# Performance work log

Hardware: AMD Instinct MI355X
Metric: run time of the kernel (lower is better)

Reference implementation:

```python
import jax, jax.numpy as jnp
import numpy as np
from jax import lax

V = 50000      # node_num
LN = 128       # feat_dim
S = 16         # stat_dim
E = 500000     # n_edges
T = 3          # propagation steps
MU = 0.9


def setup_inputs() -> dict:
    key = jax.random.key(0)
    ks = jax.random.split(key, 10)
    X_Node = jax.random.randint(ks[0], (E,), 0, V, dtype=jnp.int32)
    X_Neis = jax.random.randint(ks[1], (E,), 0, V, dtype=jnp.int32)
    dg_list = jax.random.randint(ks[2], (E,), 1, 64, dtype=jnp.int32)
    emb = jax.random.normal(ks[3], (V, LN), dtype=jnp.float32) * 0.1
    xi_w = jax.random.normal(ks[4], (2 * LN, S * S), dtype=jnp.float32) * (1.0 / np.sqrt(2 * LN))
    xi_b = jnp.zeros((S * S,), dtype=jnp.float32)
    rou_w = jax.random.normal(ks[5], (LN, S), dtype=jnp.float32) * (1.0 / np.sqrt(LN))
    rou_b = jnp.zeros((S,), dtype=jnp.float32)
    lin_w = jax.random.normal(ks[6], (LN + S, 3), dtype=jnp.float32) * (1.0 / np.sqrt(LN + S))
    lin_b = jnp.zeros((3,), dtype=jnp.float32)
    return {"X_Node": X_Node, "X_Neis": X_Neis, "dg_list": dg_list,
            "emb": emb, "xi_w": xi_w, "xi_b": xi_b,
            "rou_w": rou_w, "rou_b": rou_b, "lin_w": lin_w, "lin_b": lin_b}


def reference(X_Node, X_Neis, dg_list, emb, xi_w, xi_b, rou_w, rou_b, lin_w, lin_b):
    # edge features: concat(src embed, nbr embed) -> [E, 2*ln]
    Xn = emb[X_Node]                                  # [E, ln]
    X = jnp.concatenate([Xn, emb[X_Neis]], axis=1)    # [E, 2*ln]
    dg = dg_list.astype(emb.dtype)
    # Hw: A = Xi(X)*mu/s/dg  (constant across iterations; torch recomputes, same math)
    A = jnp.tanh(X @ xi_w + xi_b).reshape(-1, S, S)   # [E, s, s]
    A = A * (MU / S) / dg[:, None, None]
    b = jnp.tanh(Xn @ rou_w + rou_b)                  # [E, s]

    states0 = jnp.zeros((V, S), dtype=emb.dtype)

    def step(states, _):
        H = states[X_Node]                            # [E, s] gather
        H = jnp.einsum('est,et->es', A, H) + b        # per-edge small matvec
        states = jax.ops.segment_sum(H, X_Neis, num_segments=V)  # scatter-sum (AggrSum)
        return states, None

    states, _ = lax.scan(step, states0, None, length=T)
    logits = jnp.concatenate([emb, states], axis=1) @ lin_w + lin_b  # [V, 3]
    return jax.nn.softmax(logits, axis=1)
```

## Files before the change

kernel.cpp:

```cpp
#include <hip/hip_runtime.h>
#include <hip/hip_bf16.h>
#include <hip/hip_fp16.h>

#define LN_F 128

typedef __attribute__((ext_vector_type(8))) __bf16 bf16x8;
typedef __attribute__((ext_vector_type(4))) float f32x4;
typedef __attribute__((ext_vector_type(2))) _Float16 half2_t;
typedef __attribute__((ext_vector_type(2))) __fp16 fp16x2_t;

__device__ __forceinline__ unsigned short f2bf(float f) {
    unsigned u = __float_as_uint(f);
    u = u + 0x7FFFu + ((u >> 16) & 1u);
    return (unsigned short)(u >> 16);
}
__device__ __forceinline__ float tanh_polyc(float x) {
    x = fminf(1.2f, fmaxf(-1.2f, x));
    float t = x * x;
    float p = fmaf(t, -0.05396825397f, 0.13333333333f);
    p = fmaf(t, p, -0.33333333333f);
    p = fmaf(t, p, 1.0f);
    return x * p;
}
__device__ __forceinline__ float bflo(unsigned u) { return __uint_as_float(u << 16); }
__device__ __forceinline__ float bfhi(unsigned u) { return __uint_as_float(u & 0xffff0000u); }

__device__ __forceinline__ unsigned f2e5(float x) {
    unsigned short u = __half_as_ushort(__float2half(x));
    u = (unsigned short)(u + 0x7F + ((u >> 8) & 1));
    return (unsigned)(u >> 8) & 0xFFu;
}
__device__ __forceinline__ half2_t u2h2(unsigned w) {
    union { unsigned u; half2_t h; } c; c.u = w; return c.h;
}
__device__ __forceinline__ unsigned h2u(half2_t h) {
    union { half2_t h; unsigned u; } c; c.h = h; return c.u;
}
__device__ __forceinline__ unsigned pkrtz_u32(float lo, float hi) {
    union { fp16x2_t h; unsigned u; } c;
    c.h = __builtin_amdgcn_cvt_pkrtz(lo, hi);
    return c.u;
}
__device__ __forceinline__ half2_t tanh_pk(half2_t x) {
    const half2_t c2 = {(_Float16)(2.0f / 15.0f), (_Float16)(2.0f / 15.0f)};
    const half2_t c1 = {(_Float16)(-1.0f / 3.0f), (_Float16)(-1.0f / 3.0f)};
    const half2_t one = {(_Float16)1.0f, (_Float16)1.0f};
    half2_t t = x * x;
    half2_t p = t * c2 + c1;
    p = t * p + one;
    return x * p;
}

__global__ void k_conv(const float* __restrict__ emb, const float* __restrict__ xiw,
                       const float* __restrict__ rw, const int* __restrict__ Xe,
                       unsigned short* __restrict__ embb, unsigned short* __restrict__ WcT,
                       unsigned short* __restrict__ rouT, int* __restrict__ cnt,
                       float* __restrict__ B1, float* __restrict__ stB,
                       float* __restrict__ stA, int V, int E) {
    int t = blockIdx.x * blockDim.x + threadIdx.x;
    int n_emb = V * 16;
    if (t < n_emb) {
        const float4* s = (const float4*)emb;
        float4 a = s[t * 2], b = s[t * 2 + 1];
        uint4 o;
        o.x = (unsigned)f2bf(a.x) | ((unsigned)f2bf(a.y) << 16);
        o.y = (unsigned)f2bf(a.z) | ((unsigned)f2bf(a.w) << 16);
        o.z = (unsigned)f2bf(b.x) | ((unsigned)f2bf(b.y) << 16);
        o.w = (unsigned)f2bf(b.z) | ((unsigned)f2bf(b.w) << 16);
        ((uint4*)embb)[t] = o;
        B1[t] = 0.f;
        stB[t] = 0.f;
        stA[t] = 0.f;
    } else if (t < n_emb + 512 * 16) {
        int t2 = t - n_emb;
        int cp = t2 >> 4, g = t2 & 15;
        unsigned short u[8];
#pragma unroll
        for (int j = 0; j < 8; ++j) {
            int k = g * 8 + j;
            float w = (cp < 256) ? xiw[k * 256 + cp] : xiw[(128 + k) * 256 + (cp - 256)];
            u[j] = f2bf(w);
        }
        uint4 o;
        o.x = (unsigned)u[0] | ((unsigned)u[1] << 16);
        o.y = (unsigned)u[2] | ((unsigned)u[3] << 16);
        o.z = (unsigned)u[4] | ((unsigned)u[5] << 16);
        o.w = (unsigned)u[6] | ((unsigned)u[7] << 16);
        ((uint4*)WcT)[cp * 16 + (g ^ (cp & 7))] = o;
    } else if (t < n_emb + 512 * 16 + 256) {
        int t2 = t - n_emb - 512 * 16;
        int c = t2 >> 4, g = t2 & 15;
        unsigned short u[8];
#pragma unroll
        for (int j = 0; j < 8; ++j) u[j] = f2bf(rw[(g * 8 + j) * 16 + c]);
        uint4 o;
        o.x = (unsigned)u[0] | ((unsigned)u[1] << 16);
        o.y = (unsigned)u[2] | ((unsigned)u[3] << 16);
        o.z = (unsigned)u[4] | ((unsigned)u[5] << 16);
        o.w = (unsigned)u[6] | ((unsigned)u[7] << 16);
        ((uint4*)rouT)[c * 16 + (g ^ (c & 7))] = o;
    }
    if (t < E) atomicAdd(&cnt[Xe[t]], 1);
}

__global__ __launch_bounds__(256) void k_scan1(const int* __restrict__ cnt,
                                               int* __restrict__ rp,
                                               int* __restrict__ bsum, int V) {
    __shared__ int ls[256];
    int b = blockIdx.x, t = threadIdx.x;
    int i = b * 256 + t;
    int val = (i < V) ? cnt[i] : 0;
    ls[t] = val;
    __syncthreads();
    for (int off = 1; off < 256; off <<= 1) {
        int x = (t >= off) ? ls[t - off] : 0;
        __syncthreads();
        ls[t] += x;
        __syncthreads();
    }
    if (i < V) rp[i] = ls[t] - val;
    if (t == 255) bsum[b] = ls[255];
}

__global__ __launch_bounds__(256) void k_scan2(const int* __restrict__ bsum,
                                               int* __restrict__ boff, int NB) {
    __shared__ int ls[256];
    int t = threadIdx.x;
    int val = (t < NB) ? bsum[t] : 0;
    ls[t] = val;
    __syncthreads();
    for (int off = 1; off < 256; off <<= 1) {
        int x = (t >= off) ? ls[t - off] : 0;
        __syncthreads();
        ls[t] += x;
        __syncthreads();
    }
    if (t < NB) boff[t] = ls[t] - val;
}

__global__ __launch_bounds__(256) void k_permute(
    const int* __restrict__ Xn, const int* __restrict__ Xe,
    const int* __restrict__ dg, const int* __restrict__ rp,
    const int* __restrict__ boff, int* __restrict__ c2,
    uint2* __restrict__ erec, int E, int Epad, int V) {
    int part = blockIdx.x & 7;
    int sub = blockIdx.x >> 3;
    int nsub = gridDim.x >> 3;
    int per = (V + 7) >> 3;
    int vlo = part * per;
    int vhi = min(V, vlo + per);
    int stride = nsub * 256;
    for (int e = sub * 256 + threadIdx.x; e < E; e += stride) {
        int nb = Xe[e];
        if (nb >= vlo && nb < vhi) {
            int pos = rp[nb] + boff[nb >> 8] + atomicAdd(&c2[nb], 1);
            uint2 r;
            r.x = (unsigned)Xn[e] | ((unsigned)nb << 16);
            r.y = (unsigned)__float_as_int(0.05625f / (float)dg[e]);
            erec[pos] = r;
        }
    }
    if (part == 7) {
        for (int e = E + sub * 256 + threadIdx.x; e < Epad; e += stride)
            erec[e] = make_uint2(0u, 0u);
    }
}

__global__ __launch_bounds__(512) void k_U(
    const unsigned short* __restrict__ embb, const uint4* __restrict__ WcT,
    const uint4* __restrict__ rouT, const float* __restrict__ xib,
    const float* __restrict__ roub,
    unsigned* __restrict__ U8, unsigned* __restrict__ U28,
    float* __restrict__ bnode, int V) {
    __shared__ uint4 sB[2048];
    __shared__ uint4 sR[256];
    const int half = blockIdx.y;
    for (int i = threadIdx.x; i < 2048; i += 512) sB[i] = WcT[half * 2048 + i];
    if (half == 0 && threadIdx.x < 256) sR[threadIdx.x] = rouT[threadIdx.x];
    __syncthreads();

    const int wave = threadIdx.x >> 6, lane = threadIdx.x & 63;
    const int j = lane & 15, kg = lane >> 4;
    const int wbase = blockIdx.x * 512 + wave * 64;

    int nv[4];
#pragma unroll
    for (int g = 0; g < 4; ++g) nv[g] = min(wbase + g * 16 + j, V - 1);

    f32x4 acc[8][4] = {};
    f32x4 accb[4] = {};
#pragma unroll
    for (int kc = 0; kc < 4; ++kc) {
        bf16x8 bf[4];
#pragma unroll
        for (int g = 0; g < 4; ++g)
            bf[g] = *(const bf16x8*)(embb + (size_t)nv[g] * 128 + kc * 32 + kg * 8);
        int swz = (kc * 4 + kg) ^ (j & 7);
#pragma unroll
        for (int ct = 0; ct < 8; ++ct) {
            bf16x8 afr = ((const bf16x8*)sB)[(ct * 16 + j) * 16 + swz];
#pragma unroll
            for (int g = 0; g < 4; ++g)
                acc[ct][g] = __builtin_amdgcn_mfma_f32_16x16x32_bf16(afr, bf[g], acc[ct][g], 0, 0, 0);
        }
        if (half == 0) {
            bf16x8 rfr = ((const bf16x8*)sR)[j * 16 + swz];
#pragma unroll
            for (int g = 0; g < 4; ++g)
                accb[g] = __builtin_amdgcn_mfma_f32_16x16x32_bf16(rfr, bf[g], accb[g], 0, 0, 0);
        }
    }

#pragma unroll
    for (int ct = 0; ct < 8; ++ct) {
        int c0 = half * 128 + ct * 16 + kg * 4;
        float4 bias = (half < 2) ? ((const float4*)xib)[c0 >> 2]
                                 : make_float4(0.f, 0.f, 0.f, 0.f);
#pragma unroll
        for (int g = 0; g < 4; ++g) {
            int node = wbase + g * 16 + j;
            if (node < V) {
                const f32x4 a = acc[ct][g];
                float v0 = a[0] + bias.x, v1 = a[1] + bias.y;
                float v2 = a[2] + bias.z, v3 = a[3] + bias.w;
                unsigned pk = f2e5(v0) | (f2e5(v1) << 8) | (f2e5(v2) << 16) | (f2e5(v3) << 24);
                if (half < 2) U8[node * 64 + (c0 >> 2)] = pk;
                else          U28[node * 64 + ((c0 - 256) >> 2)] = pk;
            }
        }
    }
    if (half == 0) {
        float4 rb4 = ((const float4*)roub)[kg];
#pragma unroll
        for (int g = 0; g < 4; ++g) {
            int node = wbase + g * 16 + j;
            if (node < V) {
                float4 bo;
                bo.x = tanh_polyc(accb[g][0] + rb4.x);
                bo.y = tanh_polyc(accb[g][1] + rb4.y);
                bo.z = tanh_polyc(accb[g][2] + rb4.z);
                bo.w = tanh_polyc(accb[g][3] + rb4.w);
                *(float4*)(bnode + (size_t)node * 16 + kg * 4) = bo;
            }
        }
    }
}

__global__ __launch_bounds__(256) void k_B1e(
    const float* __restrict__ bnode, const uint2* __restrict__ erec,
    float* __restrict__ B1, float* __restrict__ stB, float* __restrict__ stA,
    int E, int Epad) {
    int wid = (blockIdx.x * 256 + threadIdx.x) >> 6;
    int wbase = wid * 64;
    if (wbase >= Epad) return;
    int lane = threadIdx.x & 63;
    int g = lane >> 4, s = lane & 15, lbase = g * 16;
    int sbase = wbase + lbase;

    int em = wbase + lane;
    unsigned rx = erec[em].x;
    int my_u = (int)(rx & 0xFFFFu);
    int d_own = (int)(rx >> 16);
    int d_nxt = (int)(((const unsigned*)erec)[2 * min(em + 1, Epad - 1)] >> 16);
    unsigned long long flags = __ballot(d_own != d_nxt);

    int cur = __shfl(d_own, lbase, 64);
    float acc = 0.f;
#pragma unroll 4
    for (int j = 0; j < 16; ++j) {
        int p = sbase + j;
        int u = __shfl(my_u, lbase + j, 64);
        float v = bnode[(size_t)u * 16 + s];
        acc += (p < E) ? v : 0.f;
        bool flush = ((flags >> (lbase + j)) & 1ull) || (j == 15);
        if (flush) {
            size_t idx = (size_t)cur * 16 + s;
            atomicAdd(&B1[idx], acc);
            atomicAdd(&stB[idx], acc);
            atomicAdd(&stA[idx], acc);
            acc = 0.f;
            if (j < 15) cur = __shfl(d_nxt, lbase + j, 64);
        }
    }
}

__global__ __launch_bounds__(256) void k_prop_e(
    const unsigned* __restrict__ U8, const unsigned* __restrict__ U28,
    const uint2* __restrict__ erec, const float* __restrict__ sp,
    float* __restrict__ sn, int Epad) {
    int wid = (blockIdx.x * 256 + threadIdx.x) >> 6;
    int wbase = wid * 64;
    if (wbase >= Epad) return;
    int lane = threadIdx.x & 63;
    int g = lane >> 4, s = lane & 15, lbase = g * 16;

    int em = wbase + lane;
    uint2 myr = erec[em];
    int my_u = (int)(myr.x & 0xFFFFu);
    int d_own = (int)(myr.x >> 16);
    int d_nxt = (int)(((const unsigned*)erec)[2 * min(em + 1, Epad - 1)] >> 16);
    unsigned long long flags = __ballot(d_own != d_nxt);

    int cur = __shfl(d_own, lbase, 64);
    half2_t u2h[8];
    {
        uint4 r = ((const uint4*)U28)[cur * 16 + s];
        unsigned wr[4] = {r.x, r.y, r.z, r.w};
#pragma unroll
        for (int q = 0; q < 4; ++q) {
            u2h[2 * q]     = u2h2(__builtin_amdgcn_perm(wr[q], 0u, 0x05000400u));
            u2h[2 * q + 1] = u2h2(__builtin_amdgcn_perm(wr[q], 0u, 0x07000600u));
        }
    }

    float acc = 0.f;
#pragma unroll 4
    for (int j = 0; j < 16; ++j) {
        int u = __shfl(my_u, lbase + j, 64);
        float sc = __int_as_float(__shfl((int)myr.y, lbase + j, 64));
        uint4 q1 = ((const uint4*)U8)[u * 16 + s];
        float2 hf = *(const float2*)(sp + (size_t)u * 16 + (s & 7) * 2);
        unsigned h2 = pkrtz_u32(hf.x, hf.y);
        unsigned wq[4] = {q1.x, q1.y, q1.z, q1.w};
        float sum = 0.f;
#pragma unroll
        for (int q = 0; q < 4; ++q) {
            half2_t x0 = u2h2(__builtin_amdgcn_perm(wq[q], 0u, 0x05000400u)) + u2h[2 * q];
            half2_t x1 = u2h2(__builtin_amdgcn_perm(wq[q], 0u, 0x07000600u)) + u2h[2 * q + 1];
            half2_t r0 = tanh_pk(x0);
            half2_t r1 = tanh_pk(x1);
            unsigned hm0 = __shfl(h2, lbase + 2 * q, 64);
            unsigned hm1 = __shfl(h2, lbase + 2 * q + 1, 64);
            sum = __builtin_amdgcn_fdot2(r0, u2h2(hm0), sum, false);
            sum = __builtin_amdgcn_fdot2(r1, u2h2(hm1), sum, false);
        }
        acc = fmaf(sc, sum, acc);
        bool flush = ((flags >> (lbase + j)) & 1ull) || (j == 15);
        if (flush) {
            atomicAdd(&sn[(size_t)cur * 16 + s], acc);
            acc = 0.f;
            if (j < 15) {
                cur = __shfl(d_nxt, lbase + j, 64);
                uint4 r = ((const uint4*)U28)[cur * 16 + s];
                unsigned wr[4] = {r.x, r.y, r.z, r.w};
#pragma unroll
                for (int q = 0; q < 4; ++q) {
                    u2h[2 * q]     = u2h2(__builtin_amdgcn_perm(wr[q], 0u, 0x05000400u));
                    u2h[2 * q + 1] = u2h2(__builtin_amdgcn_perm(wr[q], 0u, 0x07000600u));
                }
            }
        }
    }
}

__global__ void k_final(const unsigned short* __restrict__ embb, const float* __restrict__ st,
                        const float* __restrict__ lw, const float* __restrict__ lb,
                        float* __restrict__ out, int nv) {
    __shared__ float sw[435];
    for (int i = threadIdx.x; i < 435; i += 256) sw[i] = (i < 432) ? lw[i] : lb[i - 432];
    __syncthreads();
    int t = blockIdx.x * blockDim.x + threadIdx.x;
    int v = t >> 4, j = t & 15;
    if (v >= nv) return;
    const uint4 q = *(const uint4*)(embb + (size_t)v * 128 + j * 8);
    unsigned uu[4] = {q.x, q.y, q.z, q.w};
    float a0 = 0.f, a1 = 0.f, a2 = 0.f;
#pragma unroll
    for (int m = 0; m < 4; ++m) {
        int i = j * 8 + 2 * m;
        float x0 = bflo(uu[m]), x1 = bfhi(uu[m]);
        a0 += x0 * sw[i * 3] + x1 * sw[(i + 1) * 3];
        a1 += x0 * sw[i * 3 + 1] + x1 * sw[(i + 1) * 3 + 1];
        a2 += x0 * sw[i * 3 + 2] + x1 * sw[(i + 1) * 3 + 2];
    }
    float xs = st[(size_t)v * 16 + j];
    a0 += xs * sw[(128 + j) * 3]; a1 += xs * sw[(128 + j) * 3 + 1]; a2 += xs * sw[(128 + j) * 3 + 2];
#pragma unroll
    for (int m = 1; m < 16; m <<= 1) {
        a0 += __shfl_xor(a0, m, 64);
        a1 += __shfl_xor(a1, m, 64);
        a2 += __shfl_xor(a2, m, 64);
    }
    if (j == 0) {
        a0 += sw[432]; a1 += sw[433]; a2 += sw[434];
        float mx = fmaxf(a0, fmaxf(a1, a2));
        float e0 = __expf(a0 - mx), e1 = __expf(a1 - mx), e2 = __expf(a2 - mx);
        float inv = 1.f / (e0 + e1 + e2);
        out[(size_t)v * 3 + 0] = e0 * inv;
        out[(size_t)v * 3 + 1] = e1 * inv;
        out[(size_t)v * 3 + 2] = e2 * inv;
    }
}

extern "C" void kernel_launch(void* const* d_in, const int* in_sizes, int n_in,
                              void* d_out, int out_size, void* d_ws, size_t ws_size,
                              hipStream_t stream) {
    const int*   Xn  = (const int*)d_in[0];
    const int*   Xe  = (const int*)d_in[1];
    const int*   dg  = (const int*)d_in[2];
    const float* emb = (const float*)d_in[3];
    const float* xiw = (const float*)d_in[4];
    const float* xib = (const float*)d_in[5];
    const float* rw  = (const float*)d_in[6];
    const float* rb  = (const float*)d_in[7];
    const float* lw  = (const float*)d_in[8];
    const float* lb  = (const float*)d_in[9];
    float* out = (float*)d_out;
    const int E = in_sizes[0];
    const int V = in_sizes[3] / LN_F;
    const int NB = (V + 255) / 256;
    const int Epad = (E + 63) & ~63;

    char* p = (char*)d_ws;
    auto carve = [&](size_t bytes) {
        char* q = p; p += (bytes + 255) & ~(size_t)255; return q;
    };
    int*   cnt   = (int*)carve((size_t)V * 4);
    int*   c2    = (int*)carve((size_t)V * 4);
    size_t zero_bytes = (size_t)(p - (char*)cnt);
    float* B1    = (float*)carve((size_t)V * 16 * 4);
    unsigned short* embb = (unsigned short*)carve((size_t)V * 128 * 2);
    unsigned* U8    = (unsigned*)carve((size_t)V * 256);
    unsigned* U28   = (unsigned*)carve((size_t)V * 256);
    uint4* WcT   = (uint4*)carve(512 * 16 * 16);
    uint4* rouT  = (uint4*)carve(4096);
    float* bnode = (float*)carve((size_t)V * 16 * 4);
    float* stB   = (float*)carve((size_t)V * 16 * 4);
    float* stA   = (float*)carve((size_t)V * 16 * 4);
    int*   rp    = (int*)carve((size_t)(V + 1) * 4);
    int*   bsum  = (int*)carve(256 * 4);
    int*   boff  = (int*)carve(256 * 4);
    uint2* erec  = (uint2*)carve((size_t)Epad * 8);

    hipMemsetAsync(cnt, 0, zero_bytes, stream);

    {
        int nconv = V * 16 + 512 * 16 + 256;
        int ntot = nconv > E ? nconv : E;
        k_conv<<<(ntot + 255) / 256, 256, 0, stream>>>(
            emb, xiw, rw, Xe, embb, (unsigned short*)WcT, (unsigned short*)rouT,
            cnt, B1, stB, stA, V, E);
    }

    k_scan1<<<NB, 256, 0, stream>>>(cnt, rp, bsum, V);
    k_scan2<<<1, 256, 0, stream>>>(bsum, boff, NB);

    k_permute<<<1024, 256, 0, stream>>>(Xn, Xe, dg, rp, boff, c2, erec, E, Epad, V);

    {
        dim3 g((V + 511) / 512, 4);
        k_U<<<g, 512, 0, stream>>>(embb, WcT, rouT, xib, rb, U8, U28, bnode, V);
    }

    const int pblocks = (Epad / 64 + 3) / 4;

    k_B1e<<<pblocks, 256, 0, stream>>>(bnode, erec, B1, stB, stA, E, Epad);

    k_prop_e<<<pblocks, 256, 0, stream>>>(U8, U28, erec, B1, stB, Epad);

    k_prop_e<<<pblocks, 256, 0, stream>>>(U8, U28, erec, stB, stA, Epad);

    k_final<<<((size_t)V * 16 + 255) / 256, 256, 0, stream>>>(embb, stA, lw, lb, out, V);
}
```

Measured before the change: 178.6 us.

## Fuse block-offset scan and edge permute into node GEMM kernel launch

Merges k_scan2, k_permute and k_U into one heterogeneous launch. The first UBLOCKS blocks compute the per-node GEMM. The remaining 512 blocks each redo the small block-sum scan in shared memory and then scatter edges into CSR order. This removes two kernel launches and lets the memory-bound permute run alongside the MFMA-bound GEMM. In exchange every permute block repeats the scan, the shared-memory footprint grows for all blocks, and permute now uses 512-thread blocks.

```diff
diff --git a/kernel.cpp b/kernel.cpp
--- a/kernel.cpp
+++ b/kernel.cpp
@@ -32,9 +32,6 @@
 }
 __device__ __forceinline__ half2_t u2h2(unsigned w) {
     union { unsigned u; half2_t h; } c; c.u = w; return c.h;
-}
-__device__ __forceinline__ unsigned h2u(half2_t h) {
-    union { half2_t h; unsigned u; } c; c.h = h; return c.u;
 }
 __device__ __forceinline__ unsigned pkrtz_u32(float lo, float hi) {
     union { fp16x2_t h; unsigned u; } c;
@@ -122,126 +119,125 @@
     if (t == 255) bsum[b] = ls[255];
 }
 
-__global__ __launch_bounds__(256) void k_scan2(const int* __restrict__ bsum,
-                                               int* __restrict__ boff, int NB) {
-    __shared__ int ls[256];
-    int t = threadIdx.x;
-    int val = (t < NB) ? bsum[t] : 0;
-    ls[t] = val;
-    __syncthreads();
-    for (int off = 1; off < 256; off <<= 1) {
-        int x = (t >= off) ? ls[t - off] : 0;
-        __syncthreads();
-        ls[t] += x;
-        __syncthreads();
-    }
-    if (t < NB) boff[t] = ls[t] - val;
-}
-
-__global__ __launch_bounds__(256) void k_permute(
-    const int* __restrict__ Xn, const int* __restrict__ Xe,
-    const int* __restrict__ dg, const int* __restrict__ rp,
-    const int* __restrict__ boff, int* __restrict__ c2,
-    uint2* __restrict__ erec, int E, int Epad, int V) {
-    int part = blockIdx.x & 7;
-    int sub = blockIdx.x >> 3;
-    int nsub = gridDim.x >> 3;
-    int per = (V + 7) >> 3;
-    int vlo = part * per;
-    int vhi = min(V, vlo + per);
-    int stride = nsub * 256;
-    for (int e = sub * 256 + threadIdx.x; e < E; e += stride) {
-        int nb = Xe[e];
-        if (nb >= vlo && nb < vhi) {
-            int pos = rp[nb] + boff[nb >> 8] + atomicAdd(&c2[nb], 1);
-            uint2 r;
-            r.x = (unsigned)Xn[e] | ((unsigned)nb << 16);
-            r.y = (unsigned)__float_as_int(0.05625f / (float)dg[e]);
-            erec[pos] = r;
-        }
-    }
-    if (part == 7) {
-        for (int e = E + sub * 256 + threadIdx.x; e < Epad; e += stride)
-            erec[e] = make_uint2(0u, 0u);
-    }
-}
-
-__global__ __launch_bounds__(512) void k_U(
+__global__ __launch_bounds__(512) void k_Uperm(
     const unsigned short* __restrict__ embb, const uint4* __restrict__ WcT,
     const uint4* __restrict__ rouT, const float* __restrict__ xib,
     const float* __restrict__ roub,
     unsigned* __restrict__ U8, unsigned* __restrict__ U28,
-    float* __restrict__ bnode, int V) {
-    __shared__ uint4 sB[2048];
-    __shared__ uint4 sR[256];
-    const int half = blockIdx.y;
-    for (int i = threadIdx.x; i < 2048; i += 512) sB[i] = WcT[half * 2048 + i];
-    if (half == 0 && threadIdx.x < 256) sR[threadIdx.x] = rouT[threadIdx.x];
-    __syncthreads();
-
-    const int wave = threadIdx.x >> 6, lane = threadIdx.x & 63;
-    const int j = lane & 15, kg = lane >> 4;
-    const int wbase = blockIdx.x * 512 + wave * 64;
-
-    int nv[4];
-#pragma unroll
-    for (int g = 0; g < 4; ++g) nv[g] = min(wbase + g * 16 + j, V - 1);
-
-    f32x4 acc[8][4] = {};
-    f32x4 accb[4] = {};
-#pragma unroll
-    for (int kc = 0; kc < 4; ++kc) {
-        bf16x8 bf[4];
-#pragma unroll
-        for (int g = 0; g < 4; ++g)
-            bf[g] = *(const bf16x8*)(embb + (size_t)nv[g] * 128 + kc * 32 + kg * 8);
-        int swz = (kc * 4 + kg) ^ (j & 7);
+    float* __restrict__ bnode,
+    const int* __restrict__ Xn, const int* __restrict__ Xe,
+    const int* __restrict__ dg, const int* __restrict__ rp,
+    const int* __restrict__ bsum, int* __restrict__ c2,
+    uint2* __restrict__ erec,
+    int V, int E, int Epad, int NB, int UBLOCKS) {
+    if ((int)blockIdx.x < UBLOCKS) {
+        __shared__ uint4 sB[2048];
+        __shared__ uint4 sR[256];
+        const int half = blockIdx.x & 3;
+        for (int i = threadIdx.x; i < 2048; i += 512) sB[i] = WcT[half * 2048 + i];
+        if (half == 0 && threadIdx.x < 256) sR[threadIdx.x] = rouT[threadIdx.x];
+        __syncthreads();
+
+        const int wave = threadIdx.x >> 6, lane = threadIdx.x & 63;
+        const int j = lane & 15, kg = lane >> 4;
+        const int wbase = (blockIdx.x >> 2) * 512 + wave * 64;
+
+        int nv[4];
+#pragma unroll
+        for (int g = 0; g < 4; ++g) nv[g] = min(wbase + g * 16 + j, V - 1);
+
+        f32x4 acc[8][4] = {};
+        f32x4 accb[4] = {};
+#pragma unroll
+        for (int kc = 0; kc < 4; ++kc) {
+            bf16x8 bf[4];
+#pragma unroll
+            for (int g = 0; g < 4; ++g)
+                bf[g] = *(const bf16x8*)(embb + (size_t)nv[g] * 128 + kc * 32 + kg * 8);
+            int swz = (kc * 4 + kg) ^ (j & 7);
+#pragma unroll
+            for (int ct = 0; ct < 8; ++ct) {
+                bf16x8 afr = ((const bf16x8*)sB)[(ct * 16 + j) * 16 + swz];
+#pragma unroll
+                for (int g = 0; g < 4; ++g)
+                    acc[ct][g] = __builtin_amdgcn_mfma_f32_16x16x32_bf16(afr, bf[g], acc[ct][g], 0, 0, 0);
+            }
+            if (half == 0) {
+                bf16x8 rfr = ((const bf16x8*)sR)[j * 16 + swz];
+#pragma unroll
+                for (int g = 0; g < 4; ++g)
+                    accb[g] = __builtin_amdgcn_mfma_f32_16x16x32_bf16(rfr, bf[g], accb[g], 0, 0, 0);
+            }
+        }
+
 #pragma unroll
         for (int ct = 0; ct < 8; ++ct) {
-            bf16x8 afr = ((const bf16x8*)sB)[(ct * 16 + j) * 16 + swz];
-#pragma unroll
-            for (int g = 0; g < 4; ++g)
-                acc[ct][g] = __builtin_amdgcn_mfma_f32_16x16x32_bf16(afr, bf[g], acc[ct][g], 0, 0, 0);
+            int c0 = half * 128 + ct * 16 + kg * 4;
+            float4 bias = (half < 2) ? ((const float4*)xib)[c0 >> 2]
+                                     : make_float4(0.f, 0.f, 0.f, 0.f);
+#pragma unroll
+            for (int g = 0; g < 4; ++g) {
+                int node = wbase + g * 16 + j;
+                if (node < V) {
+                    const f32x4 a = acc[ct][g];
+                    float v0 = a[0] + bias.x, v1 = a[1] + bias.y;
+                    float v2 = a[2] + bias.z, v3 = a[3] + bias.w;
+                    unsigned pk = f2e5(v0) | (f2e5(v1) << 8) | (f2e5(v2) << 16) | (f2e5(v3) << 24);
+                    if (half < 2) U8[node * 64 + (c0 >> 2)] = pk;
+                    else          U28[node * 64 + ((c0 - 256) >> 2)] = pk;
+                }
+            }
         }
         if (half == 0) {
-            bf16x8 rfr = ((const bf16x8*)sR)[j * 16 + swz];
-#pragma unroll
-            for (int g = 0; g < 4; ++g)
-                accb[g] = __builtin_amdgcn_mfma_f32_16x16x32_bf16(rfr, bf[g], accb[g], 0, 0, 0);
-        }
-    }
-
-#pragma unroll
-    for (int ct = 0; ct < 8; ++ct) {
-        int c0 = half * 128 + ct * 16 + kg * 4;
-        float4 bias = (half < 2) ? ((const float4*)xib)[c0 >> 2]
-                                 : make_float4(0.f, 0.f, 0.f, 0.f);
-#pragma unroll
-        for (int g = 0; g < 4; ++g) {
-            int node = wbase + g * 16 + j;
-            if (node < V) {
-                const f32x4 a = acc[ct][g];
-                float v0 = a[0] + bias.x, v1 = a[1] + bias.y;
-                float v2 = a[2] + bias.z, v3 = a[3] + bias.w;
-                unsigned pk = f2e5(v0) | (f2e5(v1) << 8) | (f2e5(v2) << 16) | (f2e5(v3) << 24);
-                if (half < 2) U8[node * 64 + (c0 >> 2)] = pk;
-                else          U28[node * 64 + ((c0 - 256) >> 2)] = pk;
-            }
-        }
-    }
-    if (half == 0) {
-        float4 rb4 = ((const float4*)roub)[kg];
-#pragma unroll
-        for (int g = 0; g < 4; ++g) {
-            int node = wbase + g * 16 + j;
-            if (node < V) {
-                float4 bo;
-                bo.x = tanh_polyc(accb[g][0] + rb4.x);
-                bo.y = tanh_polyc(accb[g][1] + rb4.y);
-                bo.z = tanh_polyc(accb[g][2] + rb4.z);
-                bo.w = tanh_polyc(accb[g][3] + rb4.w);
-                *(float4*)(bnode + (size_t)node * 16 + kg * 4) = bo;
-            }
+            float4 rb4 = ((const float4*)roub)[kg];
+#pragma unroll
+            for (int g = 0; g < 4; ++g) {
+                int node = wbase + g * 16 + j;
+                if (node < V) {
+                    float4 bo;
+                    bo.x = tanh_polyc(accb[g][0] + rb4.x);
+                    bo.y = tanh_polyc(accb[g][1] + rb4.y);
+                    bo.z = tanh_polyc(accb[g][2] + rb4.z);
+                    bo.w = tanh_polyc(accb[g][3] + rb4.w);
+                    *(float4*)(bnode + (size_t)node * 16 + kg * 4) = bo;
+                }
+            }
+        }
+    } else {
+        __shared__ int lb[256];
+        int t = threadIdx.x;
+        int val = 0;
+        if (t < 256) { val = (t < NB) ? bsum[t] : 0; lb[t] = val; }
+        __syncthreads();
+        for (int off = 1; off < 256; off <<= 1) {
+            int x = (t < 256 && t >= off) ? lb[t - off] : 0;
+            __syncthreads();
+            if (t < 256) lb[t] += x;
+            __syncthreads();
+        }
+        if (t < 256) lb[t] -= val;
+        __syncthreads();
+
+        int pb = blockIdx.x - UBLOCKS;
+        int part = pb & 7, sub = pb >> 3;
+        int nsub = ((int)gridDim.x - UBLOCKS) >> 3;
+        int per = (V + 7) >> 3;
+        int vlo = part * per;
+        int vhi = min(V, vlo + per);
+        int stride = nsub * 512;
+        for (int e = sub * 512 + t; e < E; e += stride) {
+            int nb = Xe[e];
+            if (nb >= vlo && nb < vhi) {
+                int pos = rp[nb] + lb[nb >> 8] + atomicAdd(&c2[nb], 1);
+                uint2 r;
+                r.x = (unsigned)Xn[e] | ((unsigned)nb << 16);
+                r.y = (unsigned)__float_as_int(0.05625f / (float)dg[e]);
+                erec[pos] = r;
+            }
+        }
+        if (part == 7) {
+            for (int e = E + sub * 512 + t; e < Epad; e += stride)
+                erec[e] = make_uint2(0u, 0u);
         }
     }
 }
@@ -429,7 +425,6 @@
     float* stA   = (float*)carve((size_t)V * 16 * 4);
     int*   rp    = (int*)carve((size_t)(V + 1) * 4);
     int*   bsum  = (int*)carve(256 * 4);
-    int*   boff  = (int*)carve(256 * 4);
     uint2* erec  = (uint2*)carve((size_t)Epad * 8);
 
     hipMemsetAsync(cnt, 0, zero_bytes, stream);
@@ -443,13 +438,13 @@
     }
 
     k_scan1<<<NB, 256, 0, stream>>>(cnt, rp, bsum, V);
-    k_scan2<<<1, 256, 0, stream>>>(bsum, boff, NB);
-
-    k_permute<<<1024, 256, 0, stream>>>(Xn, Xe, dg, rp, boff, c2, erec, E, Epad, V);
 
     {
-        dim3 g((V + 511) / 512, 4);
-        k_U<<<g, 512, 0, stream>>>(embb, WcT, rouT, xib, rb, U8, U28, bnode, V);
+        int UBLOCKS = ((V + 511) / 512) * 4;
+        int PB = 512;
+        k_Uperm<<<UBLOCKS + PB, 512, 0, stream>>>(
+            embb, WcT, rouT, xib, rb, U8, U28, bnode,
+            Xn, Xe, dg, rp, bsum, c2, erec, V, E, Epad, NB, UBLOCKS);
     }
 
     const int pblocks = (Epad / 64 + 3) / 4;
```

After: 180.1 us. Within noise of the previous version (+0.8%).
